# Performance work log

Hardware: AMD Instinct MI355X
Metric: run time of the kernel (lower is better)

Reference implementation:

```python
import jax, jax.numpy as jnp
import numpy as np

DIM = 512; H = 56; W = 56; HEADS = 16; WS = 7; SHIFT = 3; MLP_RATIO = 4.0; B = 16
N = WS * WS              # tokens per window = 49
NW = (H // WS) * (W // WS)  # 64 windows
HID = int(DIM * MLP_RATIO)


def _rel_pos_index():
    coords = np.stack(np.meshgrid(np.arange(WS), np.arange(WS), indexing='ij')).reshape(2, -1)
    rel = (coords[:, :, None] - coords[:, None, :]).transpose(1, 2, 0)
    rel[..., 0] += WS - 1
    rel[..., 1] += WS - 1
    rel[..., 0] *= 2 * WS - 1
    return rel.sum(-1).astype(np.int32)  # (N, N)


def _attn_mask():
    # standard SW-MSA mask: 0 within same region, -100 across regions
    img = np.zeros((H, W), np.float32)
    cnt = 0
    sl = (slice(0, -WS), slice(-WS, -SHIFT), slice(-SHIFT, None))
    for hs in sl:
        for ws_ in sl:
            img[hs, ws_] = cnt
            cnt += 1
    mw = img.reshape(H // WS, WS, W // WS, WS).transpose(0, 2, 1, 3).reshape(-1, N)  # (NW, N)
    am = mw[:, None, :] - mw[:, :, None]
    return np.where(am != 0, np.float32(-100.0), np.float32(0.0))  # (NW, N, N)


def setup_inputs() -> dict:
    key = jax.random.key(0)
    ks = jax.random.split(key, 6)
    s = jnp.float32(0.02)
    return {
        'x': jax.random.normal(ks[0], (B, H * W, DIM), jnp.float32),
        'qkv_w': jax.random.normal(ks[1], (3 * DIM, DIM), jnp.float32) * s,  # layout (h dh 3) x C
        'qkv_b': jnp.zeros((3 * DIM,), jnp.float32),
        'out_w': jax.random.normal(ks[2], (DIM, DIM), jnp.float32) * s,
        'out_b': jnp.zeros((DIM,), jnp.float32),
        'rp_bias_table': jax.random.normal(ks[3], ((2 * WS - 1) ** 2, HEADS), jnp.float32) * s,
        'fc1_w': jax.random.normal(ks[4], (HID, DIM), jnp.float32) * s,
        'fc1_b': jnp.zeros((HID,), jnp.float32),
        'fc2_w': jax.random.normal(ks[5], (DIM, HID), jnp.float32) * s,
        'fc2_b': jnp.zeros((DIM,), jnp.float32),
        'ln1_w': jnp.ones((DIM,), jnp.float32),
        'ln1_b': jnp.zeros((DIM,), jnp.float32),
        'ln2_w': jnp.ones((DIM,), jnp.float32),
        'ln2_b': jnp.zeros((DIM,), jnp.float32),
        'attn_mask': jnp.asarray(_attn_mask()),
        'rp_index': jnp.asarray(_rel_pos_index()),
    }


def _ln(x, w, b):
    m = x.mean(-1, keepdims=True)
    v = ((x - m) ** 2).mean(-1, keepdims=True)
    return (x - m) * jax.lax.rsqrt(v + 1e-5) * w + b


def reference(x, qkv_w, qkv_b, out_w, out_b, rp_bias_table, fc1_w, fc1_b, fc2_w, fc2_b,
              ln1_w, ln1_b, ln2_w, ln2_b, attn_mask, rp_index):
    Bx, L, C = x.shape
    dh = C // HEADS
    scale = jnp.float32(dh) ** -0.5

    shortcut = x
    y = _ln(x, ln1_w, ln1_b).reshape(Bx, H, W, C)
    y = jnp.roll(y, (-SHIFT, -SHIFT), axis=(1, 2))
    # window partition -> (B*NW, N, C)
    xw = y.reshape(Bx, H // WS, WS, W // WS, WS, C).transpose(0, 1, 3, 2, 4, 5).reshape(-1, N, C)

    qkv = (xw @ qkv_w.T + qkv_b).reshape(-1, N, HEADS, dh, 3).transpose(4, 0, 2, 1, 3)
    q, k, v = qkv[0] * scale, qkv[1], qkv[2]          # (B_, h, N, dh)
    attn = jnp.einsum('bhnd,bhmd->bhnm', q, k)        # (B_, h, N, N)

    bias = rp_bias_table[rp_index.reshape(-1)].reshape(N, N, HEADS).transpose(2, 0, 1)
    attn = attn + 2.0 * bias                          # source adds the bias twice (faithful)
    attn = attn.reshape(Bx, NW, HEADS, N, N) + attn_mask[None, :, None]
    attn = jax.nn.softmax(attn, axis=-1).reshape(-1, HEADS, N, N)

    o = jnp.einsum('bhnm,bhmd->bhnd', attn, v).transpose(0, 2, 1, 3).reshape(-1, N, C)
    o = o @ out_w.T + out_b
    # window reverse + roll back
    o = o.reshape(Bx, H // WS, W // WS, WS, WS, C).transpose(0, 1, 3, 2, 4, 5).reshape(Bx, H, W, C)
    o = jnp.roll(o, (SHIFT, SHIFT), axis=(1, 2)).reshape(Bx, L, C)

    x = shortcut + o
    h2 = _ln(x, ln2_w, ln2_b)
    h2 = jax.nn.gelu(h2 @ fc1_w.T + fc1_b, approximate=False) @ fc2_w.T + fc2_b
    return x + h2
```

## Files before the change

kernel.cpp:

```cpp
#include <hip/hip_runtime.h>
#include <hip/hip_bf16.h>

#define CDIM 512
#define NHEADS 16
#define DH 32
#define NTOK 49
#define NWIN 64
#define BATCH 16
#define HH 56
#define WW 56
#define LTOK 3136
#define TTOK 50176
#define HID 2048
#define SHIFT_ 3

typedef short bf16x8 __attribute__((ext_vector_type(8)));
typedef float f32x4 __attribute__((ext_vector_type(4)));

__device__ __forceinline__ float b2f(unsigned int u) {
    return __uint_as_float((u & 0xffffu) << 16);
}
__device__ __forceinline__ unsigned short f2b(float f) {
    __hip_bfloat16 h = __float2bfloat16(f);
    return *reinterpret_cast<unsigned short*>(&h);
}
__device__ __forceinline__ void load8(const unsigned short* p, float* f) {
    uint4 r = *reinterpret_cast<const uint4*>(p);
    f[0] = b2f(r.x); f[1] = b2f(r.x >> 16);
    f[2] = b2f(r.y); f[3] = b2f(r.y >> 16);
    f[4] = b2f(r.z); f[5] = b2f(r.z >> 16);
    f[6] = b2f(r.w); f[7] = b2f(r.w >> 16);
}
__device__ __forceinline__ uint4 pack8(const float* f) {
    uint4 r;
    r.x = (unsigned)f2b(f[0]) | ((unsigned)f2b(f[1]) << 16);
    r.y = (unsigned)f2b(f[2]) | ((unsigned)f2b(f[3]) << 16);
    r.z = (unsigned)f2b(f[4]) | ((unsigned)f2b(f[5]) << 16);
    r.w = (unsigned)f2b(f[6]) | ((unsigned)f2b(f[7]) << 16);
    return r;
}
__device__ __forceinline__ bool probe_f32(const unsigned* p) { return p[0] == 0x3F800000u; }
__device__ __forceinline__ float ld1(const void* p, size_t i, bool f32) {
    return f32 ? ((const float*)p)[i] : b2f(((const unsigned short*)p)[i]);
}
__device__ __forceinline__ void load8_any(const void* p, size_t idx, bool f32, float* f) {
    if (f32) {
        const float4* q = (const float4*)((const float*)p + idx);
        float4 a = q[0], b = q[1];
        f[0]=a.x; f[1]=a.y; f[2]=a.z; f[3]=a.w; f[4]=b.x; f[5]=b.y; f[6]=b.z; f[7]=b.w;
    } else {
        load8((const unsigned short*)p + idx, f);
    }
}

#define GLOAD_LDS16(g, l) \
    __builtin_amdgcn_global_load_lds( \
        (const __attribute__((address_space(1))) unsigned int*)(g), \
        (__attribute__((address_space(3))) unsigned int*)(l), 16, 0, 0)

__global__ __launch_bounds__(256)
void cvt_kernel(const void* __restrict__ in, unsigned short* __restrict__ out,
                const unsigned* __restrict__ probe)
{
    bool f32in = probe_f32(probe);
    size_t idx = ((size_t)blockIdx.x * 256 + threadIdx.x) * 8;
    float f[8];
    load8_any(in, idx, f32in, f);
    *reinterpret_cast<uint4*>(out + idx) = pack8(f);
}

__global__ __launch_bounds__(256)
void cvt_qkvw_kernel(const void* __restrict__ in, unsigned short* __restrict__ out,
                     const unsigned* __restrict__ probe)
{
    bool f32in = probe_f32(probe);
    int r = blockIdx.x * 4 + (threadIdx.x >> 6);
    int lane = threadIdx.x & 63;
    int s = r >> 9, q = r & 511, h = q >> 5, d = q & 31;
    int orow = h * 96 + d * 3 + s;
    float f[8];
    load8_any(in, (size_t)orow * CDIM + lane * 8, f32in, f);
    *reinterpret_cast<uint4*>(out + (size_t)r * CDIM + lane * 8) = pack8(f);
}

__global__ __launch_bounds__(256)
void cmb_kernel(const void* __restrict__ rp_tab, const int* __restrict__ rp_idx,
                const void* __restrict__ mask, unsigned short* __restrict__ cmb,
                const unsigned* __restrict__ probe)
{
    bool f32in = probe_f32(probe);
    int wh = blockIdx.x;
    int wi = wh >> 4, h = wh & 15;
    for (int e = threadIdx.x; e < 4096; e += 256) {
        int q = e >> 6, k = e & 63;
        float v = -1e30f;
        if (q < NTOK && k < NTOK) {
            int bi = rp_idx[q * NTOK + k];
            v = 2.0f * ld1(rp_tab, (size_t)bi * NHEADS + h, f32in)
              + ld1(mask, (size_t)wi * NTOK * NTOK + (size_t)q * NTOK + k, f32in);
        }
        cmb[(size_t)wh * 4096 + e] = f2b(v);
    }
}

template<int SHIFTED, int XRAW>
__global__ __launch_bounds__(256)
void ln_kernel(const void* __restrict__ xin,
               const void* __restrict__ gw,
               const void* __restrict__ gb,
               unsigned short* __restrict__ out,
               const unsigned* __restrict__ probe)
{
    bool f32in = probe_f32(probe);
    int wid = threadIdx.x >> 6, lane = threadIdx.x & 63;
    int tok = blockIdx.x * 4 + wid;
    int c0 = lane * 8;
    float xs[8];
    load8_any(xin, (size_t)tok * CDIM + c0, XRAW && f32in, xs);
    float s = 0.f, s2 = 0.f;
#pragma unroll
    for (int j = 0; j < 8; ++j) { s += xs[j]; s2 += xs[j] * xs[j]; }
#pragma unroll
    for (int off = 32; off; off >>= 1) { s += __shfl_xor(s, off); s2 += __shfl_xor(s2, off); }
    float mean = s * (1.0f / CDIM);
    float var = s2 * (1.0f / CDIM) - mean * mean;
    float rstd = rsqrtf(var + 1e-5f);
    float wv[8], bv[8], ov[8];
    load8_any(gw, c0, f32in, wv);
    load8_any(gb, c0, f32in, bv);
#pragma unroll
    for (int j = 0; j < 8; ++j) ov[j] = (xs[j] - mean) * rstd * wv[j] + bv[j];
    size_t dst;
    if (SHIFTED) {
        int b = tok / LTOK, l = tok % LTOK;
        int h = l / WW, w = l % WW;
        int hs = (h + HH - SHIFT_) % HH;
        int ws_ = (w + WW - SHIFT_) % WW;
        int wh = hs / 7, ii = hs % 7, wwi = ws_ / 7, jj = ws_ % 7;
        int t = (b * NWIN + wh * 8 + wwi) * NTOK + ii * 7 + jj;
        dst = (size_t)t * CDIM + c0;
    } else {
        dst = (size_t)tok * CDIM + c0;
    }
    *reinterpret_cast<uint4*>(out + dst) = pack8(ov);
}

template<int EPI>
__global__ __launch_bounds__(512, 2)
void gemm_kernel(const unsigned short* __restrict__ A,
                 const unsigned short* __restrict__ Wbf,
                 const void* __restrict__ bias,
                 const void* __restrict__ aux,
                 void* __restrict__ out0,
                 unsigned short* __restrict__ out1,
                 unsigned short* __restrict__ out2,
                 int K, int moff,
                 const unsigned* __restrict__ probe)
{
    bool f32in = probe_f32(probe);
    __shared__ __align__(16) char lds[131072];
    int tid = threadIdx.x;
    int wave = tid >> 6, lane = tid & 63, quad = lane >> 4, l16 = lane & 15;

    int nbn = gridDim.x;
    int nwg = nbn * gridDim.y;
    int wg = blockIdx.y * nbn + blockIdx.x;
    int q8 = nwg >> 3, r8 = nwg & 7;
    int xcd = wg & 7, lin = wg >> 3;
    int swz = (xcd < r8 ? xcd * (q8 + 1) : r8 * (q8 + 1) + (xcd - r8) * q8) + lin;
    int bn = swz % nbn, bm = swz / nbn;

    int wm = (wave >> 2) * 128;
    int wn = (wave & 3) * 64;

    int arow = tid >> 3;
    int scol = (((tid & 7) ^ ((tid >> 3) & 7)) << 3);
    const unsigned short* aP = A   + (size_t)(bm * 256 + arow) * K + scol;
    const unsigned short* bP = Wbf + (size_t)(bn * 256 + arow) * K + scol;

    f32x4 acc[32];
#pragma unroll
    for (int t = 0; t < 32; ++t) acc[t] = (f32x4){0.f, 0.f, 0.f, 0.f};

#define STAGE(bufoff, k0) do { \
        char* dA_ = lds + (bufoff) + tid * 16; \
        char* dB_ = dA_ + 32768; \
        _Pragma("unroll") \
        for (int p_ = 0; p_ < 4; ++p_) { \
            GLOAD_LDS16(aP + (size_t)p_ * 64 * K + (k0), dA_ + p_ * 8192); \
            GLOAD_LDS16(bP + (size_t)p_ * 64 * K + (k0), dB_ + p_ * 8192); \
        } \
    } while (0)

    const int NT = K >> 6;
    STAGE(0, 0);
    __syncthreads();

    int cur = 0;
    for (int t = 0; t < NT; ++t) {
        if (t + 1 < NT) STAGE((cur ^ 1) << 16, (t + 1) << 6);
        const unsigned short* cA = (const unsigned short*)(lds + (cur << 16));
        const unsigned short* cB = (const unsigned short*)(lds + (cur << 16) + 32768);
#pragma unroll
        for (int ks = 0; ks < 2; ++ks) {
            int swzc = (((ks << 2) + quad) ^ (l16 & 7)) << 3;
            bf16x8 af[8], bfr[4];
#pragma unroll
            for (int am = 0; am < 8; ++am)
                af[am] = *reinterpret_cast<const bf16x8*>(&cA[(wm + am * 16 + l16) * 64 + swzc]);
#pragma unroll
            for (int j = 0; j < 4; ++j)
                bfr[j] = *reinterpret_cast<const bf16x8*>(&cB[(wn + j * 16 + l16) * 64 + swzc]);
#pragma unroll
            for (int am = 0; am < 8; ++am)
#pragma unroll
                for (int j = 0; j < 4; ++j)
                    acc[am * 4 + j] = __builtin_amdgcn_mfma_f32_16x16x32_bf16(
                        af[am], bfr[j], acc[am * 4 + j], 0, 0, 0);
        }
        __syncthreads();
        cur ^= 1;
    }
#undef STAGE

#pragma unroll
    for (int j = 0; j < 4; ++j) {
        int gn = bn * 256 + wn + j * 16 + l16;
        if (EPI == 0) {
            int s = gn >> 9, h = (gn >> 5) & 15, d = gn & 31;
            float bv = ld1(bias, h * 96 + d * 3 + s, f32in);
            unsigned short* outp = (s == 0) ? (unsigned short*)out0 : (s == 1 ? out1 : out2);
            float mul = (s == 0) ? 0.17677669529663687f : 1.0f;
#pragma unroll
            for (int am = 0; am < 8; ++am) {
#pragma unroll
                for (int r = 0; r < 4; ++r) {
                    int gm = bm * 256 + wm + am * 16 + quad * 4 + r;
                    int w = gm / NTOK, n = gm - w * NTOK;
                    size_t dst = ((size_t)(w * NHEADS + h) * NTOK + n) * DH + d;
                    outp[dst] = f2b((acc[am * 4 + j][r] + bv) * mul);
                }
            }
        } else {
            float bv = ld1(bias, gn, f32in);
#pragma unroll
            for (int am = 0; am < 8; ++am) {
#pragma unroll
                for (int r = 0; r < 4; ++r) {
                    int gm = bm * 256 + wm + am * 16 + quad * 4 + r;
                    float v = acc[am * 4 + j][r] + bv;
                    if (EPI == 1) {
                        int w = gm / NTOK, n = gm - w * NTOK;
                        int b = w >> 6, wi = w & 63;
                        int wh = wi >> 3, wwi = wi & 7;
                        int ii = n / 7, jj = n - ii * 7;
                        int h_ = (wh * 7 + ii + SHIFT_) % HH;
                        int w_ = (wwi * 7 + jj + SHIFT_) % WW;
                        size_t dst = ((size_t)b * LTOK + h_ * WW + w_) * CDIM + gn;
                        v += ld1(aux, dst, f32in);
                        ((unsigned short*)out0)[dst] = f2b(v);
                    } else if (EPI == 2) {
                        float g = 0.5f * v * (1.0f + erff(v * 0.70710678118654752f));
                        ((unsigned short*)out0)[(size_t)gm * HID + gn] = f2b(g);
                    } else {
                        size_t dst = (size_t)(moff + gm) * CDIM + gn;
                        v += b2f(((const unsigned short*)aux)[dst]);
                        if (f32in) ((float*)out0)[dst] = v;
                        else       ((unsigned short*)out0)[dst] = f2b(v);
                    }
                }
            }
        }
    }
}

__global__ __launch_bounds__(256)
void attn_kernel(const unsigned short* __restrict__ Qb,
                 const unsigned short* __restrict__ Kb,
                 const unsigned short* __restrict__ Vb,
                 const unsigned short* __restrict__ cmb,
                 unsigned short* __restrict__ Ob)
{
    __shared__ __align__(16) unsigned short Pl[4][64 * 72];
    int wid = threadIdx.x >> 6, lane = threadIdx.x & 63;
    int l16 = lane & 15, quad = lane >> 4;
    int wi = blockIdx.x >> 6, rem = blockIdx.x & 63;
    int b = rem >> 2, hq = rem & 3;
    int h = hq * 4 + wid;
    int bw = b * NWIN + wi;
    size_t base = (size_t)(bw * NHEADS + h) * (NTOK * DH);
    const unsigned short* cmbp = cmb + (size_t)(wi * NHEADS + h) * 4096;

    bf16x8 kf[4], qf[4];
#pragma unroll
    for (int t = 0; t < 4; ++t) {
        kf[t] = *reinterpret_cast<const bf16x8*>(Kb + base + (t * 16 + l16) * DH + quad * 8);
        qf[t] = *reinterpret_cast<const bf16x8*>(Qb + base + (t * 16 + l16) * DH + quad * 8);
    }
    f32x4 s[4][4];
#pragma unroll
    for (int kt = 0; kt < 4; ++kt)
#pragma unroll
        for (int nt = 0; nt < 4; ++nt)
            s[kt][nt] = (f32x4){0.f, 0.f, 0.f, 0.f};
#pragma unroll
    for (int kt = 0; kt < 4; ++kt)
#pragma unroll
        for (int nt = 0; nt < 4; ++nt)
            s[kt][nt] = __builtin_amdgcn_mfma_f32_16x16x32_bf16(kf[kt], qf[nt], s[kt][nt], 0, 0, 0);

    float mx[4] = {-1e30f, -1e30f, -1e30f, -1e30f}, sm[4] = {0.f, 0.f, 0.f, 0.f};
#pragma unroll
    for (int kt = 0; kt < 4; ++kt)
#pragma unroll
        for (int nt = 0; nt < 4; ++nt) {
            uint2 cv = *reinterpret_cast<const uint2*>(cmbp + (nt * 16 + l16) * 64 + kt * 16 + quad * 4);
            float c[4] = {b2f(cv.x), b2f(cv.x >> 16), b2f(cv.y), b2f(cv.y >> 16)};
#pragma unroll
            for (int r = 0; r < 4; ++r) {
                float sv = s[kt][nt][r] + c[r];
                s[kt][nt][r] = sv;
                mx[nt] = fmaxf(mx[nt], sv);
            }
        }
#pragma unroll
    for (int nt = 0; nt < 4; ++nt) {
        mx[nt] = fmaxf(mx[nt], __shfl_xor(mx[nt], 16));
        mx[nt] = fmaxf(mx[nt], __shfl_xor(mx[nt], 32));
    }
#pragma unroll
    for (int kt = 0; kt < 4; ++kt)
#pragma unroll
        for (int nt = 0; nt < 4; ++nt)
#pragma unroll
            for (int r = 0; r < 4; ++r) {
                float pv = expf(s[kt][nt][r] - mx[nt]);
                s[kt][nt][r] = pv;
                sm[nt] += pv;
            }
    float rs[4];
#pragma unroll
    for (int nt = 0; nt < 4; ++nt) {
        sm[nt] += __shfl_xor(sm[nt], 16);
        sm[nt] += __shfl_xor(sm[nt], 32);
        rs[nt] = 1.0f / sm[nt];
    }
    unsigned short* P = Pl[wid];
#pragma unroll
    for (int kt = 0; kt < 4; ++kt)
#pragma unroll
        for (int nt = 0; nt < 4; ++nt) {
            uint2 w;
            w.x = (unsigned)f2b(s[kt][nt][0] * rs[nt]) | ((unsigned)f2b(s[kt][nt][1] * rs[nt]) << 16);
            w.y = (unsigned)f2b(s[kt][nt][2] * rs[nt]) | ((unsigned)f2b(s[kt][nt][3] * rs[nt]) << 16);
            *reinterpret_cast<uint2*>(&P[(nt * 16 + l16) * 72 + kt * 16 + quad * 4]) = w;
        }

    f32x4 o[4][2];
#pragma unroll
    for (int mt = 0; mt < 4; ++mt)
#pragma unroll
        for (int n2 = 0; n2 < 2; ++n2)
            o[mt][n2] = (f32x4){0.f, 0.f, 0.f, 0.f};
#pragma unroll
    for (int ks = 0; ks < 2; ++ks) {
        bf16x8 pf[4];
#pragma unroll
        for (int mt = 0; mt < 4; ++mt)
            pf[mt] = *reinterpret_cast<const bf16x8*>(&P[(mt * 16 + l16) * 72 + ks * 32 + quad * 8]);
        bf16x8 vf[2];
#pragma unroll
        for (int n2 = 0; n2 < 2; ++n2) {
            union { bf16x8 v; unsigned short u[8]; } t;
#pragma unroll
            for (int j = 0; j < 8; ++j)
                t.u[j] = Vb[base + (size_t)(ks * 32 + quad * 8 + j) * DH + n2 * 16 + l16];
            vf[n2] = t.v;
        }
#pragma unroll
        for (int mt = 0; mt < 4; ++mt)
#pragma unroll
            for (int n2 = 0; n2 < 2; ++n2)
                o[mt][n2] = __builtin_amdgcn_mfma_f32_16x16x32_bf16(pf[mt], vf[n2], o[mt][n2], 0, 0, 0);
    }
#pragma unroll
    for (int mt = 0; mt < 4; ++mt)
#pragma unroll
        for (int n2 = 0; n2 < 2; ++n2)
#pragma unroll
            for (int r = 0; r < 4; ++r) {
                int q = mt * 16 + quad * 4 + r;
                if (q < NTOK)
                    Ob[((size_t)bw * NTOK + q) * CDIM + h * DH + n2 * 16 + l16] = f2b(o[mt][n2][r]);
            }
}

extern "C" void kernel_launch(void* const* d_in, const int* in_sizes, int n_in,
                              void* d_out, int out_size, void* d_ws, size_t ws_size,
                              hipStream_t stream)
{
    const void* x      = d_in[0];
    const void* qkv_w  = d_in[1];
    const void* qkv_b  = d_in[2];
    const void* out_w  = d_in[3];
    const void* out_b  = d_in[4];
    const void* rp_tab = d_in[5];
    const void* fc1_w  = d_in[6];
    const void* fc1_b  = d_in[7];
    const void* fc2_w  = d_in[8];
    const void* fc2_b  = d_in[9];
    const void* ln1_w  = d_in[10];
    const void* ln1_b  = d_in[11];
    const void* ln2_w  = d_in[12];
    const void* ln2_b  = d_in[13];
    const void* amask  = d_in[14];
    const int*  rp_idx = (const int*)d_in[15];
    const unsigned* probe = (const unsigned*)ln1_w;

    unsigned short* ws = (unsigned short*)d_ws;
    const size_t SZ = (size_t)TTOK * CDIM;
    unsigned short* xw = ws;
    unsigned short* Qb = ws + SZ;
    unsigned short* Kb = ws + 2 * SZ;
    unsigned short* Vb = ws + 3 * SZ;
    unsigned short* Ob = ws + 4 * SZ;
    unsigned short* Cmb = ws;
    unsigned short* X1 = ws;
    unsigned short* Hb = ws + SZ;
    unsigned short* fc1wbf = ws + 3 * SZ;
    unsigned short* fc2wbf = ws + 3 * SZ + (size_t)HID * CDIM;
    unsigned short* L2 = ws + 4 * SZ;
    unsigned short* qkvwbf = (unsigned short*)d_out;
    unsigned short* outwbf = qkvwbf + (size_t)3 * CDIM * CDIM;
    if (ws_size < 5 * SZ * sizeof(unsigned short)) return;

    const int HM = TTOK / 2;

    cvt_qkvw_kernel<<<(3 * CDIM) / 4, 256, 0, stream>>>(qkv_w, qkvwbf, probe);
    cvt_kernel<<<(CDIM * CDIM) / 2048, 256, 0, stream>>>(out_w, outwbf, probe);

    ln_kernel<1, 1><<<TTOK / 4, 256, 0, stream>>>(x, ln1_w, ln1_b, xw, probe);
    gemm_kernel<0><<<dim3((3 * CDIM) / 256, TTOK / 256), 512, 0, stream>>>(
        xw, qkvwbf, qkv_b, nullptr, Qb, Kb, Vb, CDIM, 0, probe);
    cmb_kernel<<<1024, 256, 0, stream>>>(rp_tab, rp_idx, amask, Cmb, probe);
    attn_kernel<<<4096, 256, 0, stream>>>(Qb, Kb, Vb, Cmb, Ob);

    cvt_kernel<<<(HID * CDIM) / 2048, 256, 0, stream>>>(fc1_w, fc1wbf, probe);
    cvt_kernel<<<(HID * CDIM) / 2048, 256, 0, stream>>>(fc2_w, fc2wbf, probe);

    gemm_kernel<1><<<dim3(CDIM / 256, TTOK / 256), 512, 0, stream>>>(
        Ob, outwbf, out_b, x, X1, nullptr, nullptr, CDIM, 0, probe);
    ln_kernel<0, 0><<<TTOK / 4, 256, 0, stream>>>(X1, ln2_w, ln2_b, L2, probe);

    for (int half = 0; half < 2; ++half) {
        size_t mo = (size_t)half * HM;
        gemm_kernel<2><<<dim3(HID / 256, HM / 256), 512, 0, stream>>>(
            L2 + mo * CDIM, fc1wbf, fc1_b, nullptr, Hb, nullptr, nullptr, CDIM, 0, probe);
        gemm_kernel<3><<<dim3(CDIM / 256, HM / 256), 512, 0, stream>>>(
            Hb, fc2wbf, fc2_b, X1, d_out, nullptr, nullptr, HID, (int)mo, probe);
    }
}
```

Baseline: 1.044 ms.

## Split GEMM main loop into four phases with interleaved async loads and priority

Replaces the simple double-buffered GEMM loop with a four-phase schedule. Each phase reads part of the A/B fragments from LDS, issues part of the next tile's global-to-LDS loads, then runs a block of MFMAs at raised wave priority. A is prefetched two tiles ahead into the buffer being consumed, and explicit vmcnt/lgkmcnt waits plus barriers replace __syncthreads. The aim is to overlap memory traffic with matrix math more finely, at the cost of more barriers and delicate hand-managed wait counts that could cause races if miscounted.

```diff
diff --git a/kernel.cpp b/kernel.cpp
--- a/kernel.cpp
+++ b/kernel.cpp
@@ -182,46 +182,97 @@
 #pragma unroll
     for (int t = 0; t < 32; ++t) acc[t] = (f32x4){0.f, 0.f, 0.f, 0.f};
 
-#define STAGE(bufoff, k0) do { \
-        char* dA_ = lds + (bufoff) + tid * 16; \
-        char* dB_ = dA_ + 32768; \
+#define STAGE2(srcP, dstBase, k0, ph) do { \
         _Pragma("unroll") \
-        for (int p_ = 0; p_ < 4; ++p_) { \
-            GLOAD_LDS16(aP + (size_t)p_ * 64 * K + (k0), dA_ + p_ * 8192); \
-            GLOAD_LDS16(bP + (size_t)p_ * 64 * K + (k0), dB_ + p_ * 8192); \
-        } \
+        for (int p_ = (ph) * 2; p_ < (ph) * 2 + 2; ++p_) \
+            GLOAD_LDS16((srcP) + (size_t)p_ * 64 * K + (k0), (dstBase) + p_ * 8192 + tid * 16); \
     } while (0)
 
+#define RD(base, row, ks) (*reinterpret_cast<const bf16x8*>( \
+        &(base)[(row) * 64 + (((((ks) << 2) + quad) ^ (l16 & 7)) << 3)]))
+
     const int NT = K >> 6;
-    STAGE(0, 0);
-    __syncthreads();
-
-    int cur = 0;
+    STAGE2(aP, lds, 0, 0);            STAGE2(aP, lds, 0, 1);
+    STAGE2(bP, lds + 32768, 0, 0);    STAGE2(bP, lds + 32768, 0, 1);
+    STAGE2(aP, lds + 65536, 64, 0);   STAGE2(aP, lds + 65536, 64, 1);
+    asm volatile("s_waitcnt vmcnt(4)" ::: "memory");
+    __builtin_amdgcn_s_barrier();
+
     for (int t = 0; t < NT; ++t) {
-        if (t + 1 < NT) STAGE((cur ^ 1) << 16, (t + 1) << 6);
-        const unsigned short* cA = (const unsigned short*)(lds + (cur << 16));
-        const unsigned short* cB = (const unsigned short*)(lds + (cur << 16) + 32768);
-#pragma unroll
-        for (int ks = 0; ks < 2; ++ks) {
-            int swzc = (((ks << 2) + quad) ^ (l16 & 7)) << 3;
-            bf16x8 af[8], bfr[4];
-#pragma unroll
-            for (int am = 0; am < 8; ++am)
-                af[am] = *reinterpret_cast<const bf16x8*>(&cA[(wm + am * 16 + l16) * 64 + swzc]);
+        const int buf = t & 1;
+        char* ldsc = lds + (buf << 16);
+        char* ldso = lds + ((buf ^ 1) << 16);
+        const unsigned short* cA = (const unsigned short*)ldsc;
+        const unsigned short* cB = (const unsigned short*)(ldsc + 32768);
+        bf16x8 af[8][2], bfr[2][4];
+
+#pragma unroll
+        for (int am = 0; am < 4; ++am) {
+            af[am][0] = RD(cA, wm + am * 16 + l16, 0);
+            af[am][1] = RD(cA, wm + am * 16 + l16, 1);
+        }
+#pragma unroll
+        for (int j = 0; j < 4; ++j) bfr[0][j] = RD(cB, wn + j * 16 + l16, 0);
+        if (t + 1 < NT) STAGE2(bP, ldso + 32768, (t + 1) << 6, 0);
+        __builtin_amdgcn_s_barrier();
+        __builtin_amdgcn_s_setprio(1);
+#pragma unroll
+        for (int am = 0; am < 4; ++am)
 #pragma unroll
             for (int j = 0; j < 4; ++j)
-                bfr[j] = *reinterpret_cast<const bf16x8*>(&cB[(wn + j * 16 + l16) * 64 + swzc]);
-#pragma unroll
-            for (int am = 0; am < 8; ++am)
-#pragma unroll
-                for (int j = 0; j < 4; ++j)
-                    acc[am * 4 + j] = __builtin_amdgcn_mfma_f32_16x16x32_bf16(
-                        af[am], bfr[j], acc[am * 4 + j], 0, 0, 0);
-        }
-        __syncthreads();
-        cur ^= 1;
-    }
-#undef STAGE
+                acc[am * 4 + j] = __builtin_amdgcn_mfma_f32_16x16x32_bf16(
+                    af[am][0], bfr[0][j], acc[am * 4 + j], 0, 0, 0);
+        __builtin_amdgcn_s_setprio(0);
+        __builtin_amdgcn_s_barrier();
+
+#pragma unroll
+        for (int am = 4; am < 8; ++am) {
+            af[am][0] = RD(cA, wm + am * 16 + l16, 0);
+            af[am][1] = RD(cA, wm + am * 16 + l16, 1);
+        }
+        if (t + 1 < NT) STAGE2(bP, ldso + 32768, (t + 1) << 6, 1);
+        __builtin_amdgcn_s_barrier();
+        __builtin_amdgcn_s_setprio(1);
+#pragma unroll
+        for (int am = 4; am < 8; ++am)
+#pragma unroll
+            for (int j = 0; j < 4; ++j)
+                acc[am * 4 + j] = __builtin_amdgcn_mfma_f32_16x16x32_bf16(
+                    af[am][0], bfr[0][j], acc[am * 4 + j], 0, 0, 0);
+        __builtin_amdgcn_s_setprio(0);
+        asm volatile("s_waitcnt lgkmcnt(0)" ::: "memory");
+        __builtin_amdgcn_s_barrier();
+
+#pragma unroll
+        for (int j = 0; j < 4; ++j) bfr[1][j] = RD(cB, wn + j * 16 + l16, 1);
+        if (t + 2 < NT) STAGE2(aP, ldsc, (t + 2) << 6, 0);
+        __builtin_amdgcn_s_barrier();
+        __builtin_amdgcn_s_setprio(1);
+#pragma unroll
+        for (int am = 0; am < 4; ++am)
+#pragma unroll
+            for (int j = 0; j < 4; ++j)
+                acc[am * 4 + j] = __builtin_amdgcn_mfma_f32_16x16x32_bf16(
+                    af[am][1], bfr[1][j], acc[am * 4 + j], 0, 0, 0);
+        __builtin_amdgcn_s_setprio(0);
+        __builtin_amdgcn_s_barrier();
+
+        if (t + 2 < NT) STAGE2(aP, ldsc, (t + 2) << 6, 1);
+        __builtin_amdgcn_s_barrier();
+        __builtin_amdgcn_s_setprio(1);
+#pragma unroll
+        for (int am = 4; am < 8; ++am)
+#pragma unroll
+            for (int j = 0; j < 4; ++j)
+                acc[am * 4 + j] = __builtin_amdgcn_mfma_f32_16x16x32_bf16(
+                    af[am][1], bfr[1][j], acc[am * 4 + j], 0, 0, 0);
+        __builtin_amdgcn_s_setprio(0);
+        if (t + 2 < NT)      asm volatile("s_waitcnt vmcnt(4)" ::: "memory");
+        else if (t + 1 < NT) asm volatile("s_waitcnt vmcnt(0)" ::: "memory");
+        __builtin_amdgcn_s_barrier();
+    }
+#undef STAGE2
+#undef RD
 
 #pragma unroll
     for (int j = 0; j < 4; ++j) {
```

Measured after the change: 1.056 ms. About the same (+1.1%).
